# Kernel tuning notes

Measured on AMD Instinct MI355X. Metric: run time of the kernel, lower is better.

The kernel has to match this reference:

```python
import jax, jax.numpy as jnp
import numpy as np

IOU_THRESHOLD = 0.5
EPS = 1e-7  # ultralytics bbox_iou eps


def _bbox_iou_xywh(b1, b2):
    # b1, b2: broadcastable [..., 4] in (cx, cy, w, h) format (ultralytics default xywh=True)
    x1, y1, w1, h1 = b1[..., 0], b1[..., 1], b1[..., 2], b1[..., 3]
    x2, y2, w2, h2 = b2[..., 0], b2[..., 1], b2[..., 2], b2[..., 3]
    b1x1, b1x2 = x1 - w1 * 0.5, x1 + w1 * 0.5
    b1y1, b1y2 = y1 - h1 * 0.5, y1 + h1 * 0.5
    b2x1, b2x2 = x2 - w2 * 0.5, x2 + w2 * 0.5
    b2y1, b2y2 = y2 - h2 * 0.5, y2 + h2 * 0.5
    iw = jnp.clip(jnp.minimum(b1x2, b2x2) - jnp.maximum(b1x1, b2x1), 0.0)
    ih = jnp.clip(jnp.minimum(b1y2, b2y2) - jnp.maximum(b1y1, b2y1), 0.0)
    inter = iw * ih
    union = w1 * h1 + w2 * h2 - inter + EPS
    return inter / union


def setup_inputs() -> dict:
    key = jax.random.key(0)
    k1, k2, k3, k4, k5 = jax.random.split(key, 5)
    N, R, M, C = 2048, 10, 2048, 84
    xy = jax.random.uniform(k1, (N, 2), minval=0.0, maxval=1000.0)
    wh = jax.random.uniform(k2, (N, 2), minval=30.0, maxval=80.0)
    boxes = jnp.concatenate([xy, wh], axis=-1)                      # [N, 4] xywh
    pred = jnp.concatenate([boxes, jax.random.uniform(k3, (N, C - 4))], axis=-1)  # [N, C]
    # dropout runs: same boxes with ~1px jitter -> IoU > 0.5 guaranteed (realistic MC-dropout)
    dropout_preds = boxes[None, :, :] + jax.random.normal(k4, (R, M, 4))          # [R, M, 4]
    dropout_cls_confs = jax.nn.softmax(jax.random.normal(k5, (R, M, C)), axis=-1)  # [R, M, C]
    return {"pred": pred, "dropout_preds": dropout_preds, "dropout_cls_confs": dropout_cls_confs}


def reference(pred, dropout_preds, dropout_cls_confs):
    # pred: [N, C] (first 4 cols = xywh box); dropout_preds: [R, M, 4]; dropout_cls_confs: [R, M, C]
    R = dropout_preds.shape[0]
    iou = _bbox_iou_xywh(pred[:, None, None, :4], dropout_preds[None, :, :, :])  # [N, R, M]
    hit = iou > IOU_THRESHOLD                                                    # [N, R, M]
    matched = jnp.any(hit, axis=-1)                                              # [N, R]
    first_idx = jnp.argmax(hit, axis=-1)                                         # first j with iou>thr (torch break)
    # gather cls confidences of the first match per (pred, run): [N, R, C]
    conf = dropout_cls_confs[jnp.arange(R)[None, :], first_idx]
    # runs without a match contribute nothing to the entropy sum; p=1 -> -p*log(p)=0
    p = jnp.where(matched[..., None], conf, 1.0)
    entropy = -(p * jnp.log(p)).sum(axis=1)                                      # [N, C], sum over matched runs
    # faithful to torch: zero fallback row gives 0*log(0)=nan entropy
    entropy = jnp.where(jnp.any(matched, axis=1)[:, None], entropy, jnp.nan)
    sm = jax.nn.softmax(entropy, axis=-1)                                        # softmax over classes
    return (1.0 - sm).max(axis=-1)                                               # [N]
```

## Files before the change

### kernel.cpp

```cpp
#include <hip/hip_runtime.h>
#include <math.h>

#define NN 2048
#define RR 10
#define MM 2048
#define CC 84
#define IEPS 1e-7f

__global__ __launch_bounds__(256) void match_kernel(
    const float* __restrict__ pred,
    const float* __restrict__ dpreds,
    int* __restrict__ first_idx) {
  int wid = (blockIdx.x * blockDim.x + threadIdx.x) >> 6;
  int lane = threadIdx.x & 63;
  if (wid >= NN * RR) return;
  int n = wid & (NN - 1);
  int r = wid >> 11;

  float4 pb = *reinterpret_cast<const float4*>(pred + (size_t)n * CC);
  const float b1x1 = fmaf(-0.5f, pb.z, pb.x), b1x2 = fmaf(0.5f, pb.z, pb.x);
  const float b1y1 = fmaf(-0.5f, pb.w, pb.y), b1y2 = fmaf(0.5f, pb.w, pb.y);
  const float a1e = pb.z * pb.w + IEPS;

  const float4* __restrict__ dp =
      reinterpret_cast<const float4*>(dpreds + (size_t)r * MM * 4);

  int found = -1;
  for (int m0 = 0; m0 < MM; m0 += 256) {
    float4 d0 = dp[m0 + lane];
    float4 d1 = dp[m0 + 64 + lane];
    float4 d2 = dp[m0 + 128 + lane];
    float4 d3 = dp[m0 + 192 + lane];

#define HIT(db, h)                                                          \
    {                                                                       \
      float x1 = fmaf(-0.5f, db.z, db.x), x2 = fmaf(0.5f, db.z, db.x);      \
      float y1 = fmaf(-0.5f, db.w, db.y), y2 = fmaf(0.5f, db.w, db.y);      \
      float iw = fmaxf(fminf(b1x2, x2) - fmaxf(b1x1, x1), 0.0f);            \
      float ih = fmaxf(fminf(b1y2, y2) - fmaxf(b1y1, y1), 0.0f);            \
      float inter = iw * ih;                                                \
      float t = fmaf(db.z, db.w, a1e);                   \
      h = (3.0f * inter > t);                                               \
    }
    bool h0, h1, h2, h3;
    HIT(d0, h0) HIT(d1, h1) HIT(d2, h2) HIT(d3, h3)
#undef HIT

    unsigned long long b0 = __ballot(h0);
    unsigned long long b1 = __ballot(h1);
    unsigned long long b2 = __ballot(h2);
    unsigned long long b3 = __ballot(h3);
    if (b0 | b1 | b2 | b3) {
      if (b0)      found = m0 +       (__ffsll(b0) - 1);
      else if (b1) found = m0 + 64  + (__ffsll(b1) - 1);
      else if (b2) found = m0 + 128 + (__ffsll(b2) - 1);
      else         found = m0 + 192 + (__ffsll(b3) - 1);
      break;
    }
  }
  if (lane == 0) first_idx[n * RR + r] = found;
}

__global__ __launch_bounds__(256) void entropy_kernel(
    const float* __restrict__ confs,
    const int* __restrict__ first_idx,
    float* __restrict__ out) {
  int lane = threadIdx.x & 63;
  int n = blockIdx.x * (blockDim.x >> 6) + (threadIdx.x >> 6);
  if (n >= NN) return;

  int idxs[RR];
  bool anym = false;
#pragma unroll
  for (int r = 0; r < RR; ++r) {
    idxs[r] = first_idx[n * RR + r];
    anym = anym || (idxs[r] >= 0);
  }

  const bool has_hi = (lane + 64) < CC;
  float e0 = 0.0f, e1 = 0.0f;
#pragma unroll
  for (int r = 0; r < RR; ++r) {
    if (idxs[r] >= 0) {
      const float* row = confs + ((size_t)r * MM + (size_t)idxs[r]) * CC;
      float p0 = row[lane];
      e0 -= p0 * __logf(p0);
      if (has_hi) {
        float p1 = row[lane + 64];
        e1 -= p1 * __logf(p1);
      }
    }
  }

  float maxE = fmaxf(e0, has_hi ? e1 : -INFINITY);
  float minE = fminf(e0, has_hi ? e1 : INFINITY);
#pragma unroll
  for (int off = 32; off >= 1; off >>= 1) {
    maxE = fmaxf(maxE, __shfl_xor(maxE, off));
    minE = fminf(minE, __shfl_xor(minE, off));
  }
  float s = __expf(e0 - maxE) + (has_hi ? __expf(e1 - maxE) : 0.0f);
#pragma unroll
  for (int off = 32; off >= 1; off >>= 1) s += __shfl_xor(s, off);

  float result = anym ? (1.0f - __expf(minE - maxE) / s) : nanf("");
  if (lane == 0) out[n] = result;
}

extern "C" void kernel_launch(void* const* d_in, const int* in_sizes, int n_in,
                              void* d_out, int out_size, void* d_ws, size_t ws_size,
                              hipStream_t stream) {
  const float* pred   = (const float*)d_in[0];
  const float* dpreds = (const float*)d_in[1];
  const float* confs  = (const float*)d_in[2];
  float* out = (float*)d_out;
  int* first_idx = (int*)d_ws;

  {
    int total_waves = NN * RR;
    int blocks = (total_waves * 64 + 255) / 256;
    match_kernel<<<blocks, 256, 0, stream>>>(pred, dpreds, first_idx);
  }
  {
    int blocks = (NN + 3) / 4;
    entropy_kernel<<<blocks, 256, 0, stream>>>(confs, first_idx, out);
  }
}
```

Measured before the change: 23.38 us.

## Prefetch next dropout-box chunk and interleave prediction indices across waves

The match kernel now loads the next 256-box chunk of dropout predictions before testing the current one, a software prefetch meant to hide global-load latency. It also changes the wave-to-work mapping: each block handles one run and four predictions spaced 512 apart, so neighbouring blocks and waves touch different predictions instead of consecutive ones. Since matches usually occur at the prediction's own index, this spreads early exits across the block. The cost is extra registers for the prefetch and a wasted prefetch when the loop exits early.

```diff
diff --git a/kernel.cpp b/kernel.cpp
--- a/kernel.cpp
+++ b/kernel.cpp
@@ -6,16 +6,18 @@
 #define MM 2048
 #define CC 84
 #define IEPS 1e-7f
+#define JB 512
 
 __global__ __launch_bounds__(256) void match_kernel(
     const float* __restrict__ pred,
     const float* __restrict__ dpreds,
     int* __restrict__ first_idx) {
-  int wid = (blockIdx.x * blockDim.x + threadIdx.x) >> 6;
   int lane = threadIdx.x & 63;
-  if (wid >= NN * RR) return;
-  int n = wid & (NN - 1);
-  int r = wid >> 11;
+  int w = threadIdx.x >> 6;
+  int B = blockIdx.x;
+  int r = B / JB;
+  int j = B - r * JB;
+  int n = j + (w << 9);
 
   float4 pb = *reinterpret_cast<const float4*>(pred + (size_t)n * CC);
   const float b1x1 = fmaf(-0.5f, pb.z, pb.x), b1x2 = fmaf(0.5f, pb.z, pb.x);
@@ -25,12 +27,18 @@
   const float4* __restrict__ dp =
       reinterpret_cast<const float4*>(dpreds + (size_t)r * MM * 4);
 
+  float4 c0 = dp[lane];
+  float4 c1 = dp[64 + lane];
+  float4 c2 = dp[128 + lane];
+  float4 c3 = dp[192 + lane];
+
   int found = -1;
   for (int m0 = 0; m0 < MM; m0 += 256) {
-    float4 d0 = dp[m0 + lane];
-    float4 d1 = dp[m0 + 64 + lane];
-    float4 d2 = dp[m0 + 128 + lane];
-    float4 d3 = dp[m0 + 192 + lane];
+    int mb = m0 + 256 < MM ? m0 + 256 : m0;
+    float4 p0 = dp[mb + lane];
+    float4 p1 = dp[mb + 64 + lane];
+    float4 p2 = dp[mb + 128 + lane];
+    float4 p3 = dp[mb + 192 + lane];
 
 #define HIT(db, h)                                                          \
     {                                                                       \
@@ -43,7 +51,7 @@
       h = (3.0f * inter > t);                                               \
     }
     bool h0, h1, h2, h3;
-    HIT(d0, h0) HIT(d1, h1) HIT(d2, h2) HIT(d3, h3)
+    HIT(c0, h0) HIT(c1, h1) HIT(c2, h2) HIT(c3, h3)
 #undef HIT
 
     unsigned long long b0 = __ballot(h0);
@@ -57,6 +65,7 @@
       else         found = m0 + 192 + (__ffsll(b3) - 1);
       break;
     }
+    c0 = p0; c1 = p1; c2 = p2; c3 = p3;
   }
   if (lane == 0) first_idx[n * RR + r] = found;
 }
@@ -116,13 +125,6 @@
   float* out = (float*)d_out;
   int* first_idx = (int*)d_ws;
 
-  {
-    int total_waves = NN * RR;
-    int blocks = (total_waves * 64 + 255) / 256;
-    match_kernel<<<blocks, 256, 0, stream>>>(pred, dpreds, first_idx);
-  }
-  {
-    int blocks = (NN + 3) / 4;
-    entropy_kernel<<<blocks, 256, 0, stream>>>(confs, first_idx, out);
-  }
+  match_kernel<<<RR * JB, 256, 0, stream>>>(pred, dpreds, first_idx);
+  entropy_kernel<<<(NN + 3) / 4, 256, 0, stream>>>(confs, first_idx, out);
 }
```

Result: slower. 24.75 us (+5.8%).

## Bin dropout boxes by x-coordinate to prune IoU match search

Applied to the files above, without the earlier changes.

Adds a setup kernel that buckets each run's dropout boxes into x-coordinate bins with offsets and records the maximum width. The match kernel then scans only the bins that can overlap each prediction and reduces the minimum original index instead of scanning linearly with early exit. This cuts the IoU work per (prediction, run) pair, at the cost of an extra kernel launch with low parallelism and indirect index loads.

```diff
diff --git a/kernel.cpp b/kernel.cpp
--- a/kernel.cpp
+++ b/kernel.cpp
@@ -5,15 +5,74 @@
 #define RR 10
 #define MM 2048
 #define CC 84
+#define NB 64
 #define IEPS 1e-7f
+
+__device__ __forceinline__ int bin_of(float v) {
+  int b = (int)floorf(v * 0.064f);
+  return min(NB - 1, max(0, b));
+}
+
+__global__ __launch_bounds__(1024) void setup_kernel(
+    const float* __restrict__ dpreds,
+    float4* __restrict__ bbox, int* __restrict__ bidx,
+    int* __restrict__ off, float* __restrict__ maxw) {
+  __shared__ int cnt[NB];
+  __shared__ int cur[NB];
+  __shared__ unsigned wmax_sh;
+  int r = blockIdx.x;
+  int t = threadIdx.x;
+  if (t < NB) cnt[t] = 0;
+  if (t == 0) wmax_sh = 0u;
+  __syncthreads();
+
+  const float4* dp = reinterpret_cast<const float4*>(dpreds + (size_t)r * MM * 4);
+  float4 bx[MM / 1024];
+  int bn[MM / 1024];
+  float wm = 0.0f;
+#pragma unroll
+  for (int k = 0; k < MM / 1024; ++k) {
+    float4 d = dp[t + k * 1024];
+    bx[k] = d;
+    bn[k] = bin_of(d.x);
+    atomicAdd(&cnt[bn[k]], 1);
+    wm = fmaxf(wm, d.z);
+  }
+  atomicMax(&wmax_sh, __float_as_uint(wm));
+  __syncthreads();
+
+  if (t < 64) {
+    int c = cnt[t];
+    int inc = c;
+#pragma unroll
+    for (int o = 1; o < 64; o <<= 1) {
+      int x = __shfl_up(inc, o);
+      if (t >= o) inc += x;
+    }
+    cur[t] = inc - c;
+    off[r * (NB + 1) + t + 1] = inc;
+    if (t == 0) {
+      off[r * (NB + 1)] = 0;
+      maxw[r] = __uint_as_float(wmax_sh);
+    }
+  }
+  __syncthreads();
+
+#pragma unroll
+  for (int k = 0; k < MM / 1024; ++k) {
+    int slot = atomicAdd(&cur[bn[k]], 1);
+    bbox[(size_t)r * MM + slot] = bx[k];
+    bidx[(size_t)r * MM + slot] = t + k * 1024;
+  }
+}
 
 __global__ __launch_bounds__(256) void match_kernel(
     const float* __restrict__ pred,
-    const float* __restrict__ dpreds,
+    const float4* __restrict__ bbox, const int* __restrict__ bidx,
+    const int* __restrict__ off, const float* __restrict__ maxw,
     int* __restrict__ first_idx) {
   int wid = (blockIdx.x * blockDim.x + threadIdx.x) >> 6;
   int lane = threadIdx.x & 63;
-  if (wid >= NN * RR) return;
   int n = wid & (NN - 1);
   int r = wid >> 11;
 
@@ -22,43 +81,49 @@
   const float b1y1 = fmaf(-0.5f, pb.w, pb.y), b1y2 = fmaf(0.5f, pb.w, pb.y);
   const float a1e = pb.z * pb.w + IEPS;
 
-  const float4* __restrict__ dp =
-      reinterpret_cast<const float4*>(dpreds + (size_t)r * MM * 4);
+  float R = fmaf(0.5f, maxw[r], fmaf(0.5f, pb.z, 0.5f));
+  int blo = bin_of(pb.x - R);
+  int bhi = bin_of(pb.x + R);
+  int start = off[r * (NB + 1) + blo];
+  int end = off[r * (NB + 1) + bhi + 1];
+  int len = end - start;
 
-  int found = -1;
-  for (int m0 = 0; m0 < MM; m0 += 256) {
-    float4 d0 = dp[m0 + lane];
-    float4 d1 = dp[m0 + 64 + lane];
-    float4 d2 = dp[m0 + 128 + lane];
-    float4 d3 = dp[m0 + 192 + lane];
+  const float4* __restrict__ bb = bbox + (size_t)r * MM;
+  const int* __restrict__ bi = bidx + (size_t)r * MM;
 
-#define HIT(db, h)                                                          \
+  int best = 0x7FFFFFFF;
+  for (int base = 0; base < len; base += 256) {
+    int last = len - 1;
+    int i0 = base + lane;
+    int c0 = start + min(i0, last);
+    int c1 = start + min(i0 + 64, last);
+    int c2 = start + min(i0 + 128, last);
+    int c3 = start + min(i0 + 192, last);
+    float4 d0 = bb[c0];
+    float4 d1 = bb[c1];
+    float4 d2 = bb[c2];
+    float4 d3 = bb[c3];
+
+#define HIT(db, idx, valid)                                                 \
     {                                                                       \
       float x1 = fmaf(-0.5f, db.z, db.x), x2 = fmaf(0.5f, db.z, db.x);      \
       float y1 = fmaf(-0.5f, db.w, db.y), y2 = fmaf(0.5f, db.w, db.y);      \
       float iw = fmaxf(fminf(b1x2, x2) - fmaxf(b1x1, x1), 0.0f);            \
       float ih = fmaxf(fminf(b1y2, y2) - fmaxf(b1y1, y1), 0.0f);            \
       float inter = iw * ih;                                                \
-      float t = fmaf(db.z, db.w, a1e);                   \
-      h = (3.0f * inter > t);                                               \
+      float tt = fmaf(db.z, db.w, a1e);                                     \
+      if ((3.0f * inter > tt) && (valid)) best = min(best, bi[idx]);        \
     }
-    bool h0, h1, h2, h3;
-    HIT(d0, h0) HIT(d1, h1) HIT(d2, h2) HIT(d3, h3)
+    HIT(d0, c0, i0 < len)
+    HIT(d1, c1, i0 + 64 < len)
+    HIT(d2, c2, i0 + 128 < len)
+    HIT(d3, c3, i0 + 192 < len)
 #undef HIT
+  }
 
-    unsigned long long b0 = __ballot(h0);
-    unsigned long long b1 = __ballot(h1);
-    unsigned long long b2 = __ballot(h2);
-    unsigned long long b3 = __ballot(h3);
-    if (b0 | b1 | b2 | b3) {
-      if (b0)      found = m0 +       (__ffsll(b0) - 1);
-      else if (b1) found = m0 + 64  + (__ffsll(b1) - 1);
-      else if (b2) found = m0 + 128 + (__ffsll(b2) - 1);
-      else         found = m0 + 192 + (__ffsll(b3) - 1);
-      break;
-    }
-  }
-  if (lane == 0) first_idx[n * RR + r] = found;
+#pragma unroll
+  for (int o = 32; o >= 1; o >>= 1) best = min(best, __shfl_xor(best, o));
+  if (lane == 0) first_idx[n * RR + r] = (best == 0x7FFFFFFF) ? -1 : best;
 }
 
 __global__ __launch_bounds__(256) void entropy_kernel(
@@ -95,13 +160,13 @@
   float maxE = fmaxf(e0, has_hi ? e1 : -INFINITY);
   float minE = fminf(e0, has_hi ? e1 : INFINITY);
 #pragma unroll
-  for (int off = 32; off >= 1; off >>= 1) {
-    maxE = fmaxf(maxE, __shfl_xor(maxE, off));
-    minE = fminf(minE, __shfl_xor(minE, off));
+  for (int o = 32; o >= 1; o >>= 1) {
+    maxE = fmaxf(maxE, __shfl_xor(maxE, o));
+    minE = fminf(minE, __shfl_xor(minE, o));
   }
   float s = __expf(e0 - maxE) + (has_hi ? __expf(e1 - maxE) : 0.0f);
 #pragma unroll
-  for (int off = 32; off >= 1; off >>= 1) s += __shfl_xor(s, off);
+  for (int o = 32; o >= 1; o >>= 1) s += __shfl_xor(s, o);
 
   float result = anym ? (1.0f - __expf(minE - maxE) / s) : nanf("");
   if (lane == 0) out[n] = result;
@@ -114,15 +179,16 @@
   const float* dpreds = (const float*)d_in[1];
   const float* confs  = (const float*)d_in[2];
   float* out = (float*)d_out;
-  int* first_idx = (int*)d_ws;
 
-  {
-    int total_waves = NN * RR;
-    int blocks = (total_waves * 64 + 255) / 256;
-    match_kernel<<<blocks, 256, 0, stream>>>(pred, dpreds, first_idx);
-  }
-  {
-    int blocks = (NN + 3) / 4;
-    entropy_kernel<<<blocks, 256, 0, stream>>>(confs, first_idx, out);
-  }
+  char* ws = (char*)d_ws;
+  float4* bbox     = (float4*)ws;
+  int*    bidx     = (int*)(ws + (size_t)RR * MM * 16);
+  int*    firstidx = bidx + RR * MM;
+  int*    off      = firstidx + NN * RR;
+  float*  maxw     = (float*)(off + RR * (NB + 1));
+
+  setup_kernel<<<RR, 1024, 0, stream>>>(dpreds, bbox, bidx, off, maxw);
+  match_kernel<<<NN * RR / 4, 256, 0, stream>>>(pred, bbox, bidx, off, maxw,
+                                                firstidx);
+  entropy_kernel<<<(NN + 3) / 4, 256, 0, stream>>>(confs, firstidx, out);
 }
```

After: 27.04 us. 15.7% more time.

## Fuse match and entropy kernels into one block-per-prediction kernel

Applied to the files above, without the earlier changes.

Merges the IoU matching and entropy kernels into a single launch with one 640-thread block per prediction, where each of the ten waves handles one dropout run. Match indices go through shared memory instead of a global workspace, which removes the second launch and the global round trip. In exchange, nine of the ten waves sit idle during the entropy phase, and the block size changes occupancy.

```diff
diff --git a/kernel.cpp b/kernel.cpp
--- a/kernel.cpp
+++ b/kernel.cpp
@@ -7,15 +7,16 @@
 #define CC 84
 #define IEPS 1e-7f
 
-__global__ __launch_bounds__(256) void match_kernel(
+__global__ __launch_bounds__(640) void fused_kernel(
     const float* __restrict__ pred,
     const float* __restrict__ dpreds,
-    int* __restrict__ first_idx) {
-  int wid = (blockIdx.x * blockDim.x + threadIdx.x) >> 6;
-  int lane = threadIdx.x & 63;
-  if (wid >= NN * RR) return;
-  int n = wid & (NN - 1);
-  int r = wid >> 11;
+    const float* __restrict__ confs,
+    float* __restrict__ out) {
+  __shared__ int sidx[RR];
+
+  const int n = blockIdx.x;
+  const int r = threadIdx.x >> 6;
+  const int lane = threadIdx.x & 63;
 
   float4 pb = *reinterpret_cast<const float4*>(pred + (size_t)n * CC);
   const float b1x1 = fmaf(-0.5f, pb.z, pb.x), b1x2 = fmaf(0.5f, pb.z, pb.x);
@@ -58,53 +59,47 @@
       break;
     }
   }
-  if (lane == 0) first_idx[n * RR + r] = found;
-}
+  if (lane == 0) sidx[r] = found;
+  __syncthreads();
 
-__global__ __launch_bounds__(256) void entropy_kernel(
-    const float* __restrict__ confs,
-    const int* __restrict__ first_idx,
-    float* __restrict__ out) {
-  int lane = threadIdx.x & 63;
-  int n = blockIdx.x * (blockDim.x >> 6) + (threadIdx.x >> 6);
-  if (n >= NN) return;
+  if (r == 0) {
+    int idxs[RR];
+    bool anym = false;
+#pragma unroll
+    for (int q = 0; q < RR; ++q) {
+      idxs[q] = sidx[q];
+      anym = anym || (idxs[q] >= 0);
+    }
 
-  int idxs[RR];
-  bool anym = false;
+    const bool has_hi = (lane + 64) < CC;
+    float e0 = 0.0f, e1 = 0.0f;
 #pragma unroll
-  for (int r = 0; r < RR; ++r) {
-    idxs[r] = first_idx[n * RR + r];
-    anym = anym || (idxs[r] >= 0);
-  }
-
-  const bool has_hi = (lane + 64) < CC;
-  float e0 = 0.0f, e1 = 0.0f;
-#pragma unroll
-  for (int r = 0; r < RR; ++r) {
-    if (idxs[r] >= 0) {
-      const float* row = confs + ((size_t)r * MM + (size_t)idxs[r]) * CC;
-      float p0 = row[lane];
-      e0 -= p0 * __logf(p0);
-      if (has_hi) {
-        float p1 = row[lane + 64];
-        e1 -= p1 * __logf(p1);
+    for (int q = 0; q < RR; ++q) {
+      if (idxs[q] >= 0) {
+        const float* row = confs + ((size_t)q * MM + (size_t)idxs[q]) * CC;
+        float p0 = row[lane];
+        e0 -= p0 * __logf(p0);
+        if (has_hi) {
+          float p1 = row[lane + 64];
+          e1 -= p1 * __logf(p1);
+        }
       }
     }
+
+    float maxE = fmaxf(e0, has_hi ? e1 : -INFINITY);
+    float minE = fminf(e0, has_hi ? e1 : INFINITY);
+#pragma unroll
+    for (int o = 32; o >= 1; o >>= 1) {
+      maxE = fmaxf(maxE, __shfl_xor(maxE, o));
+      minE = fminf(minE, __shfl_xor(minE, o));
+    }
+    float s = __expf(e0 - maxE) + (has_hi ? __expf(e1 - maxE) : 0.0f);
+#pragma unroll
+    for (int o = 32; o >= 1; o >>= 1) s += __shfl_xor(s, o);
+
+    float result = anym ? (1.0f - __expf(minE - maxE) / s) : nanf("");
+    if (lane == 0) out[n] = result;
   }
-
-  float maxE = fmaxf(e0, has_hi ? e1 : -INFINITY);
-  float minE = fminf(e0, has_hi ? e1 : INFINITY);
-#pragma unroll
-  for (int off = 32; off >= 1; off >>= 1) {
-    maxE = fmaxf(maxE, __shfl_xor(maxE, off));
-    minE = fminf(minE, __shfl_xor(minE, off));
-  }
-  float s = __expf(e0 - maxE) + (has_hi ? __expf(e1 - maxE) : 0.0f);
-#pragma unroll
-  for (int off = 32; off >= 1; off >>= 1) s += __shfl_xor(s, off);
-
-  float result = anym ? (1.0f - __expf(minE - maxE) / s) : nanf("");
-  if (lane == 0) out[n] = result;
 }
 
 extern "C" void kernel_launch(void* const* d_in, const int* in_sizes, int n_in,
@@ -114,15 +109,6 @@
   const float* dpreds = (const float*)d_in[1];
   const float* confs  = (const float*)d_in[2];
   float* out = (float*)d_out;
-  int* first_idx = (int*)d_ws;
 
-  {
-    int total_waves = NN * RR;
-    int blocks = (total_waves * 64 + 255) / 256;
-    match_kernel<<<blocks, 256, 0, stream>>>(pred, dpreds, first_idx);
-  }
-  {
-    int blocks = (NN + 3) / 4;
-    entropy_kernel<<<blocks, 256, 0, stream>>>(confs, first_idx, out);
-  }
+  fused_kernel<<<NN, 640, 0, stream>>>(pred, dpreds, confs, out);
 }
```

New measurement: 23.93 us. 2.3% more time.
